# Performance work log

Hardware: AMD Instinct MI355X
Metric: run time of the kernel (lower is better)

## Reference

```python
import math
import jax, jax.numpy as jnp
import numpy as np

EMBED = 1024
HEADS = 16
HDIM = EMBED // HEADS

def setup_inputs() -> dict:
    key = jax.random.key(0)
    ks = jax.random.split(key, 11)
    N, L, E = 2, 2048, EMBED
    s = 1.0 / math.sqrt(E)
    return {
        "q": jax.random.normal(ks[0], (N, L, E), jnp.float32),
        "k": jax.random.normal(ks[1], (N, L, E), jnp.float32),
        "v": jax.random.normal(ks[2], (N, L, E), jnp.float32),
        "Wq": jax.random.normal(ks[3], (E, E), jnp.float32) * s,
        "bq": jnp.zeros((E,), jnp.float32),
        "Wk": jax.random.normal(ks[4], (E, E), jnp.float32) * s,
        "bk": jnp.zeros((E,), jnp.float32),
        "Wv": jax.random.normal(ks[5], (E, E), jnp.float32) * s,
        "bv": jnp.zeros((E,), jnp.float32),
        "Wo": jax.random.normal(ks[6], (E, E), jnp.float32) * s,
        "bo": jnp.zeros((E,), jnp.float32),
    }

def reference(q, k, v, Wq, bq, Wk, bk, Wv, bv, Wo, bo):
    N, L, E = q.shape
    h, d = HEADS, HDIM
    # linear projections (torch Linear: x @ W.T + b)
    qh = (q @ Wq.T + bq).reshape(N, L, h, d)
    kh = (k @ Wk.T + bk).reshape(N, L, h, d)
    vh = (v @ Wv.T + bv).reshape(N, L, h, d)
    # scaled dot-product attention (dropout in eval mode -> identity)
    energy = jnp.einsum('nqhd,nkhd->nhqk', qh, kh)
    attn = jax.nn.softmax(energy / math.sqrt(d), axis=-1)
    out = jnp.einsum('nhql,nlhd->nhqd', attn, vh)
    out = out.transpose(0, 2, 1, 3).reshape(N, L, E)
    return out @ Wo.T + bo
```

## Files before the change

kernel.cpp:

```cpp
#include <hip/hip_runtime.h>
#include <hip/hip_bf16.h>
#include <math.h>

typedef unsigned short u16;
typedef unsigned int u32;
typedef u16 u16x4 __attribute__((ext_vector_type(4)));
typedef u16 u16x8 __attribute__((ext_vector_type(8)));
typedef short bf16x8 __attribute__((ext_vector_type(8)));
typedef float f32x4 __attribute__((ext_vector_type(4)));

#define LSEQ 2048
#define NH   32

#define QSCALE 0.18033688011112042f

__device__ __forceinline__ u16 f2bf(float f) {
    __hip_bfloat16 h = __float2bfloat16(f);
    union { __hip_bfloat16 h; u16 u; } c; c.h = h; return c.u;
}

__global__ __launch_bounds__(256) void cvt_bf16(
    const float* __restrict__ src, u16* __restrict__ dst, int n4)
{
    int stride = gridDim.x * 256;
    for (int i = blockIdx.x * 256 + threadIdx.x; i < n4; i += stride) {
        float4 a = ((const float4*)src)[i];
        u16x4 p;
        p[0] = f2bf(a.x); p[1] = f2bf(a.y); p[2] = f2bf(a.z); p[3] = f2bf(a.w);
        ((u16x4*)dst)[i] = p;
    }
}

__global__ __launch_bounds__(256) void cvt3_bf16(
    const float* __restrict__ s0, const float* __restrict__ s1,
    const float* __restrict__ s2, u16* __restrict__ dst)
{
    int i = blockIdx.x * 256 + threadIdx.x;
    const float* s = (i < (1 << 18)) ? s0 : (i < (2 << 18)) ? s1 : s2;
    int off = i & ((1 << 18) - 1);
    float4 a = ((const float4*)s)[off];
    u16x4 p;
    p[0] = f2bf(a.x); p[1] = f2bf(a.y); p[2] = f2bf(a.z); p[3] = f2bf(a.w);
    ((u16x4*)dst)[i] = p;
}

template<int MODE, int QS>
__global__ __launch_bounds__(256, 1) void proj_gemm4(
    const u16* __restrict__ A, const u16* __restrict__ W,
    const float* __restrict__ bias, void* __restrict__ Out)
{
    __shared__ u16 Al[2][128 * 64];
    __shared__ u16 Bl[2][128 * 64];

    const int tid  = threadIdx.x;
    const int lane = tid & 63;
    const int w    = tid >> 6;
    const int lr   = lane & 15, lg = lane >> 4;
    const int m0   = blockIdx.y * 128;
    const int n0   = blockIdx.x * 128;
    const int wr   = (w >> 1) * 64;
    const int wc   = (w & 1) * 64;
    const int srow = tid >> 3;
    const int sc8  = tid & 7;
    const int ssw  = (sc8 ^ (srow & 7)) * 8;

    f32x4 acc[4][4] = {};
    u16x8 ra[4], rb[4];

    #define LOADS(k0)                                                          \
        _Pragma("unroll")                                                      \
        for (int p_ = 0; p_ < 4; ++p_) {                                       \
            ra[p_] = *(const u16x8*)(A + (size_t)(m0 + p_ * 32 + srow) * 1024  \
                                     + (k0) + ssw);                            \
            rb[p_] = *(const u16x8*)(W + (size_t)(n0 + p_ * 32 + srow) * 1024  \
                                     + (k0) + ssw);                            \
        }
    #define WRITE(buf)                                                         \
        _Pragma("unroll")                                                      \
        for (int p_ = 0; p_ < 4; ++p_) {                                       \
            *(u16x8*)((char*)&Al[buf][0] + (p_ * 32 + srow) * 128 + sc8 * 16)  \
                = ra[p_];                                                      \
            *(u16x8*)((char*)&Bl[buf][0] + (p_ * 32 + srow) * 128 + sc8 * 16)  \
                = rb[p_];                                                      \
        }

    LOADS(0)
    WRITE(0)
    LOADS(64)
    __syncthreads();

    for (int t = 0; t < 16; ++t) {
        const int c = t & 1;
        if (t + 1 < 16) {
            WRITE(c ^ 1)
            if (t + 2 < 16) LOADS((t + 2) * 64)
        }
        const char* Ac = (const char*)&Al[c][0];
        const char* Bc = (const char*)&Bl[c][0];
        #pragma unroll
        for (int ks = 0; ks < 2; ++ks) {
            const int co = ((ks * 4 + lg) * 16) ^ ((lr & 7) << 4);
            bf16x8 af[4], bfr[4];
            #pragma unroll
            for (int i = 0; i < 4; ++i)
                af[i] = *(const bf16x8*)(Ac + (wr + i * 16 + lr) * 128 + co);
            #pragma unroll
            for (int j = 0; j < 4; ++j)
                bfr[j] = *(const bf16x8*)(Bc + (wc + j * 16 + lr) * 128 + co);
            #pragma unroll
            for (int i = 0; i < 4; ++i)
                #pragma unroll
                for (int j = 0; j < 4; ++j)
                    acc[i][j] = __builtin_amdgcn_mfma_f32_16x16x32_bf16(
                        af[i], bfr[j], acc[i][j], 0, 0, 0);
        }
        __syncthreads();
    }

    #pragma unroll
    for (int j = 0; j < 4; ++j) {
        const int nn = n0 + wc + j * 16 + lr;
        const float bj = bias[nn];
        #pragma unroll
        for (int i = 0; i < 4; ++i) {
            #pragma unroll
            for (int r = 0; r < 4; ++r) {
                const int m = m0 + wr + i * 16 + lg * 4 + r;
                float vv = acc[i][j][r] + bj;
                if (QS) vv *= QSCALE;
                if (MODE == 0) {
                    const int n = m >> 11, l = m & 2047;
                    const int h = nn >> 6, d = nn & 63;
                    ((u16*)Out)[(((size_t)(n * 16 + h) * 2048) + l) * 64 + d] = f2bf(vv);
                } else if (MODE == 1) {
                    const int n = m >> 11, l = m & 2047;
                    const int h = nn >> 6, d = nn & 63;
                    ((u16*)Out)[(((size_t)(n * 16 + h) * 64) + d) * 2048 + l] = f2bf(vv);
                } else {
                    ((float*)Out)[(size_t)m * 1024 + nn] = vv;
                }
            }
        }
    }
    #undef LOADS
    #undef WRITE
}

__global__ __launch_bounds__(256, 4) void flash_attn5(
    const u16* __restrict__ Qh, const u16* __restrict__ Kh,
    const u16* __restrict__ Vt, u16* __restrict__ Oout)
{
    const int tid  = threadIdx.x;
    const int lane = tid & 63;
    const int w    = tid >> 6;
    const int lr   = lane & 15, lg = lane >> 4;
    const int t8   = tid & 7,   td8 = tid >> 3;
    const int nh   = blockIdx.y;
    const int q0   = blockIdx.x * 64;
    const int scol = (t8 ^ (td8 & 7)) * 8;

    const u16* Qb = Qh + (size_t)nh * LSEQ * 64;
    const u16* Kb = Kh + (size_t)nh * LSEQ * 64;
    const u16* Vb = Vt + (size_t)nh * 64 * LSEQ;

    __shared__ u16 Kl[2][64 * 64];
    __shared__ u16 Vl[2][64 * 64];
    __shared__ u16 Pl[4][16 * 64];

    bf16x8 aq[2];
    #pragma unroll
    for (int ks = 0; ks < 2; ++ks)
        aq[ks] = *(const bf16x8*)(Qb +
            (size_t)(q0 + w * 16 + lr) * 64 + ks * 32 + lg * 8);

    float m_run[4], l_run[4];
    f32x4 Oacc[4] = {};
    #pragma unroll
    for (int r = 0; r < 4; ++r) { m_run[r] = -INFINITY; l_run[r] = 0.f; }

    u16x8 ldK0, ldK1, ldV0, ldV1;
    #define LOADS(s0)                                                          \
        ldK0 = *(const u16x8*)(Kb + (size_t)((s0) + td8) * 64 + scol);         \
        ldK1 = *(const u16x8*)(Kb + (size_t)((s0) + td8 + 32) * 64 + scol);    \
        ldV0 = *(const u16x8*)(Vb + (size_t)td8 * LSEQ + (s0) + scol);         \
        ldV1 = *(const u16x8*)(Vb + (size_t)(td8 + 32) * LSEQ + (s0) + scol);
    #define WRITE(buf)                                                         \
        *(u16x8*)((char*)&Kl[buf][0] + td8 * 128 + t8 * 16)        = ldK0;     \
        *(u16x8*)((char*)&Kl[buf][0] + (td8 + 32) * 128 + t8 * 16) = ldK1;     \
        *(u16x8*)((char*)&Vl[buf][0] + td8 * 128 + t8 * 16)        = ldV0;     \
        *(u16x8*)((char*)&Vl[buf][0] + (td8 + 32) * 128 + t8 * 16) = ldV1;

    LOADS(0)
    WRITE(0)
    LOADS(64)
    __syncthreads();

    for (int t = 0; t < LSEQ / 64; ++t) {
        const int c = t & 1;
        if (t + 1 < LSEQ / 64) {
            WRITE(c ^ 1)
            if (t + 2 < LSEQ / 64) LOADS((t + 2) * 64)
        }
        const char* Kc = (const char*)&Kl[c][0];
        const char* Vc = (const char*)&Vl[c][0];
        char* Pw = (char*)&Pl[w][0];

        f32x4 S[4] = {};
        #pragma unroll
        for (int ks = 0; ks < 2; ++ks) {
            const int co = ((ks * 4 + lg) * 16) ^ ((lr & 7) << 4);
            #pragma unroll
            for (int ct = 0; ct < 4; ++ct) {
                bf16x8 kb = *(const bf16x8*)(Kc + (ct * 16 + lr) * 128 + co);
                S[ct] = __builtin_amdgcn_mfma_f32_16x16x32_bf16(
                    aq[ks], kb, S[ct], 0, 0, 0);
            }
        }

        {
            float m_new[4], sf[4], rs[4];
            #pragma unroll
            for (int r = 0; r < 4; ++r) {
                float tm = fmaxf(fmaxf(S[0][r], S[1][r]), fmaxf(S[2][r], S[3][r]));
                #pragma unroll
                for (int mk = 1; mk <= 8; mk <<= 1)
                    tm = fmaxf(tm, __shfl_xor(tm, mk, 64));
                m_new[r] = fmaxf(m_run[r], tm);
                sf[r] = exp2f(m_run[r] - m_new[r]);
                m_run[r] = m_new[r];
                rs[r] = 0.f;
            }
            #pragma unroll
            for (int ct = 0; ct < 4; ++ct)
                #pragma unroll
                for (int r = 0; r < 4; ++r) {
                    float p = exp2f(S[ct][r] - m_new[r]);
                    rs[r] += p;
                    int pr = lg * 4 + r;
                    *(u16*)(Pw + pr * 128 +
                            (((ct * 16 + lr) * 2) ^ ((pr & 7) << 4))) = f2bf(p);
                }
            #pragma unroll
            for (int r = 0; r < 4; ++r) {
                float s = rs[r];
                #pragma unroll
                for (int mk = 1; mk <= 8; mk <<= 1)
                    s += __shfl_xor(s, mk, 64);
                l_run[r] = l_run[r] * sf[r] + s;
            }
            #pragma unroll
            for (int dt = 0; dt < 4; ++dt)
                #pragma unroll
                for (int r = 0; r < 4; ++r)
                    Oacc[dt][r] *= sf[r];
        }

        #pragma unroll
        for (int ks = 0; ks < 2; ++ks) {
            const int co = ((ks * 4 + lg) * 16) ^ ((lr & 7) << 4);
            bf16x8 pa = *(const bf16x8*)(Pw + lr * 128 + co);
            #pragma unroll
            for (int dt = 0; dt < 4; ++dt) {
                bf16x8 vb = *(const bf16x8*)(Vc + (dt * 16 + lr) * 128 + co);
                Oacc[dt] = __builtin_amdgcn_mfma_f32_16x16x32_bf16(
                    pa, vb, Oacc[dt], 0, 0, 0);
            }
        }
        __syncthreads();
    }
    #undef LOADS
    #undef WRITE

    const int n = nh >> 4, h = nh & 15;
    #pragma unroll
    for (int dt = 0; dt < 4; ++dt)
        #pragma unroll
        for (int r = 0; r < 4; ++r) {
            float o = Oacc[dt][r] / l_run[r];
            int qq = q0 + w * 16 + lg * 4 + r;
            Oout[((size_t)(n * LSEQ + qq)) * 1024 + h * 64 + dt * 16 + lr] = f2bf(o);
        }
}

extern "C" void kernel_launch(void* const* d_in, const int* in_sizes, int n_in,
                              void* d_out, int out_size, void* d_ws, size_t ws_size,
                              hipStream_t stream) {
    const float* q  = (const float*)d_in[0];
    const float* k  = (const float*)d_in[1];
    const float* v  = (const float*)d_in[2];
    const float* Wq = (const float*)d_in[3];
    const float* bq = (const float*)d_in[4];
    const float* Wk = (const float*)d_in[5];
    const float* bk = (const float*)d_in[6];
    const float* Wv = (const float*)d_in[7];
    const float* bv = (const float*)d_in[8];
    const float* Wo = (const float*)d_in[9];
    const float* bo = (const float*)d_in[10];

    u16* ws = (u16*)d_ws;
    u16* Qh = ws;
    u16* Kh = ws + (size_t)4 * 1024 * 1024;
    u16* Vt = ws + (size_t)8 * 1024 * 1024;
    u16* S4 = ws + (size_t)12 * 1024 * 1024;

    u16* Wb  = (u16*)d_out;
    u16* Wqb = Wb;
    u16* Wkb = Wb + (size_t)1 * 1024 * 1024;
    u16* Wvb = Wb + (size_t)2 * 1024 * 1024;

    const int n4in = (2 * LSEQ * 1024) / 4;
    dim3 cb(256);
    dim3 gg(8, 32), gb(256);

    cvt3_bf16<<<dim3(3 * 1024), cb, 0, stream>>>(Wq, Wk, Wv, Wb);
    cvt_bf16<<<dim3(2048), cb, 0, stream>>>(q, S4, n4in);
    proj_gemm4<0, 1><<<gg, gb, 0, stream>>>(S4, Wqb, bq, Qh);
    cvt_bf16<<<dim3(2048), cb, 0, stream>>>(k, S4, n4in);
    proj_gemm4<0, 0><<<gg, gb, 0, stream>>>(S4, Wkb, bk, Kh);
    cvt_bf16<<<dim3(2048), cb, 0, stream>>>(v, S4, n4in);
    proj_gemm4<1, 0><<<gg, gb, 0, stream>>>(S4, Wvb, bv, Vt);
    flash_attn5<<<dim3(LSEQ / 64, NH), gb, 0, stream>>>(Qh, Kh, Vt, S4);
    cvt_bf16<<<dim3(1024), cb, 0, stream>>>(Wo, Qh, (1 << 18));
    proj_gemm4<2, 0><<<gg, gb, 0, stream>>>(S4, Qh, bo, (float*)d_out);
}
```

Measured before the change: 309.9 us.

## Shrink GEMM N-tile and add lazy softmax rescale with MFMA row sums

The projection GEMMs move from 128x128 to 128x64 tiles with a doubled grid and a launch bound of two blocks per CU, aiming for better CU fill on 256 CUs. In the attention kernel the per-tile online-softmax rescale is skipped when no new row max exceeds the running max by more than a threshold, tested wave-uniformly with __all. The row sums come from an extra MFMA against a ones vector instead of shuffle reductions. This trades some MFMA work and weaker numerical headroom (exp values up to 2^11 in bf16 P) for fewer shuffles and exps.

```diff
diff --git a/kernel.cpp b/kernel.cpp
--- a/kernel.cpp
+++ b/kernel.cpp
@@ -45,44 +45,46 @@
 }
 
 template<int MODE, int QS>
-__global__ __launch_bounds__(256, 1) void proj_gemm4(
+__global__ __launch_bounds__(256, 2) void proj_gemm5(
     const u16* __restrict__ A, const u16* __restrict__ W,
     const float* __restrict__ bias, void* __restrict__ Out)
 {
     __shared__ u16 Al[2][128 * 64];
-    __shared__ u16 Bl[2][128 * 64];
+    __shared__ u16 Bl[2][64 * 64];
 
     const int tid  = threadIdx.x;
     const int lane = tid & 63;
     const int w    = tid >> 6;
     const int lr   = lane & 15, lg = lane >> 4;
     const int m0   = blockIdx.y * 128;
-    const int n0   = blockIdx.x * 128;
+    const int n0   = blockIdx.x * 64;
     const int wr   = (w >> 1) * 64;
-    const int wc   = (w & 1) * 64;
+    const int wc   = (w & 1) * 32;
     const int srow = tid >> 3;
     const int sc8  = tid & 7;
     const int ssw  = (sc8 ^ (srow & 7)) * 8;
 
-    f32x4 acc[4][4] = {};
-    u16x8 ra[4], rb[4];
+    f32x4 acc[4][2] = {};
+    u16x8 ra[4], rb[2];
 
     #define LOADS(k0)                                                          \
         _Pragma("unroll")                                                      \
-        for (int p_ = 0; p_ < 4; ++p_) {                                       \
+        for (int p_ = 0; p_ < 4; ++p_)                                         \
             ra[p_] = *(const u16x8*)(A + (size_t)(m0 + p_ * 32 + srow) * 1024  \
                                      + (k0) + ssw);                            \
+        _Pragma("unroll")                                                      \
+        for (int p_ = 0; p_ < 2; ++p_)                                         \
             rb[p_] = *(const u16x8*)(W + (size_t)(n0 + p_ * 32 + srow) * 1024  \
-                                     + (k0) + ssw);                            \
-        }
+                                     + (k0) + ssw);
     #define WRITE(buf)                                                         \
         _Pragma("unroll")                                                      \
-        for (int p_ = 0; p_ < 4; ++p_) {                                       \
+        for (int p_ = 0; p_ < 4; ++p_)                                         \
             *(u16x8*)((char*)&Al[buf][0] + (p_ * 32 + srow) * 128 + sc8 * 16)  \
                 = ra[p_];                                                      \
+        _Pragma("unroll")                                                      \
+        for (int p_ = 0; p_ < 2; ++p_)                                         \
             *(u16x8*)((char*)&Bl[buf][0] + (p_ * 32 + srow) * 128 + sc8 * 16)  \
-                = rb[p_];                                                      \
-        }
+                = rb[p_];
 
     LOADS(0)
     WRITE(0)
@@ -100,17 +102,17 @@
         #pragma unroll
         for (int ks = 0; ks < 2; ++ks) {
             const int co = ((ks * 4 + lg) * 16) ^ ((lr & 7) << 4);
-            bf16x8 af[4], bfr[4];
+            bf16x8 af[4], bfr[2];
             #pragma unroll
             for (int i = 0; i < 4; ++i)
                 af[i] = *(const bf16x8*)(Ac + (wr + i * 16 + lr) * 128 + co);
             #pragma unroll
-            for (int j = 0; j < 4; ++j)
+            for (int j = 0; j < 2; ++j)
                 bfr[j] = *(const bf16x8*)(Bc + (wc + j * 16 + lr) * 128 + co);
             #pragma unroll
             for (int i = 0; i < 4; ++i)
                 #pragma unroll
-                for (int j = 0; j < 4; ++j)
+                for (int j = 0; j < 2; ++j)
                     acc[i][j] = __builtin_amdgcn_mfma_f32_16x16x32_bf16(
                         af[i], bfr[j], acc[i][j], 0, 0, 0);
         }
@@ -118,7 +120,7 @@
     }
 
     #pragma unroll
-    for (int j = 0; j < 4; ++j) {
+    for (int j = 0; j < 2; ++j) {
         const int nn = n0 + wc + j * 16 + lr;
         const float bj = bias[nn];
         #pragma unroll
@@ -146,7 +148,7 @@
     #undef WRITE
 }
 
-__global__ __launch_bounds__(256, 4) void flash_attn5(
+__global__ __launch_bounds__(256, 4) void flash_attn6(
     const u16* __restrict__ Qh, const u16* __restrict__ Kh,
     const u16* __restrict__ Vt, u16* __restrict__ Oout)
 {
@@ -173,10 +175,14 @@
         aq[ks] = *(const bf16x8*)(Qb +
             (size_t)(q0 + w * 16 + lr) * 64 + ks * 32 + lg * 8);
 
-    float m_run[4], l_run[4];
-    f32x4 Oacc[4] = {};
+    const short one_bf = (short)0x3F80;
+    bf16x8 vones = { one_bf, one_bf, one_bf, one_bf,
+                     one_bf, one_bf, one_bf, one_bf };
+
+    float m_run[4];
+    f32x4 Oacc[5] = {};
     #pragma unroll
-    for (int r = 0; r < 4; ++r) { m_run[r] = -INFINITY; l_run[r] = 0.f; }
+    for (int r = 0; r < 4; ++r) m_run[r] = -INFINITY;
 
     u16x8 ldK0, ldK1, ldV0, ldV1;
     #define LOADS(s0)                                                          \
@@ -218,41 +224,42 @@
         }
 
         {
-            float m_new[4], sf[4], rs[4];
-            #pragma unroll
-            for (int r = 0; r < 4; ++r) {
-                float tm = fmaxf(fmaxf(S[0][r], S[1][r]), fmaxf(S[2][r], S[3][r]));
+            float lm = S[0][0];
+            #pragma unroll
+            for (int ct = 0; ct < 4; ++ct)
                 #pragma unroll
-                for (int mk = 1; mk <= 8; mk <<= 1)
-                    tm = fmaxf(tm, __shfl_xor(tm, mk, 64));
-                m_new[r] = fmaxf(m_run[r], tm);
-                sf[r] = exp2f(m_run[r] - m_new[r]);
-                m_run[r] = m_new[r];
-                rs[r] = 0.f;
+                for (int r = 0; r < 4; ++r)
+                    lm = fmaxf(lm, S[ct][r]);
+            #pragma unroll
+            for (int mk = 1; mk <= 8; mk <<= 1)
+                lm = fmaxf(lm, __shfl_xor(lm, mk, 64));
+            float mmin = fminf(fminf(m_run[0], m_run[1]),
+                               fminf(m_run[2], m_run[3]));
+            if (!__all((int)(lm <= mmin + 11.0f))) {
+                #pragma unroll
+                for (int r = 0; r < 4; ++r) {
+                    float tm = fmaxf(fmaxf(S[0][r], S[1][r]),
+                                     fmaxf(S[2][r], S[3][r]));
+                    #pragma unroll
+                    for (int mk = 1; mk <= 8; mk <<= 1)
+                        tm = fmaxf(tm, __shfl_xor(tm, mk, 64));
+                    float mn = fmaxf(m_run[r], tm);
+                    float sf = exp2f(m_run[r] - mn);
+                    m_run[r] = mn;
+                    #pragma unroll
+                    for (int dt = 0; dt < 5; ++dt)
+                        Oacc[dt][r] *= sf;
+                }
             }
             #pragma unroll
             for (int ct = 0; ct < 4; ++ct)
                 #pragma unroll
                 for (int r = 0; r < 4; ++r) {
-                    float p = exp2f(S[ct][r] - m_new[r]);
-                    rs[r] += p;
+                    float p = exp2f(S[ct][r] - m_run[r]);
                     int pr = lg * 4 + r;
                     *(u16*)(Pw + pr * 128 +
                             (((ct * 16 + lr) * 2) ^ ((pr & 7) << 4))) = f2bf(p);
                 }
-            #pragma unroll
-            for (int r = 0; r < 4; ++r) {
-                float s = rs[r];
-                #pragma unroll
-                for (int mk = 1; mk <= 8; mk <<= 1)
-                    s += __shfl_xor(s, mk, 64);
-                l_run[r] = l_run[r] * sf[r] + s;
-            }
-            #pragma unroll
-            for (int dt = 0; dt < 4; ++dt)
-                #pragma unroll
-                for (int r = 0; r < 4; ++r)
-                    Oacc[dt][r] *= sf[r];
         }
 
         #pragma unroll
@@ -265,6 +272,8 @@
                 Oacc[dt] = __builtin_amdgcn_mfma_f32_16x16x32_bf16(
                     pa, vb, Oacc[dt], 0, 0, 0);
             }
+            Oacc[4] = __builtin_amdgcn_mfma_f32_16x16x32_bf16(
+                pa, vones, Oacc[4], 0, 0, 0);
         }
         __syncthreads();
     }
@@ -276,7 +285,7 @@
     for (int dt = 0; dt < 4; ++dt)
         #pragma unroll
         for (int r = 0; r < 4; ++r) {
-            float o = Oacc[dt][r] / l_run[r];
+            float o = Oacc[dt][r] / Oacc[4][r];
             int qq = q0 + w * 16 + lg * 4 + r;
             Oout[((size_t)(n * LSEQ + qq)) * 1024 + h * 64 + dt * 16 + lr] = f2bf(o);
         }
@@ -310,16 +319,16 @@
 
     const int n4in = (2 * LSEQ * 1024) / 4;
     dim3 cb(256);
-    dim3 gg(8, 32), gb(256);
+    dim3 gg(16, 32), gb(256);
 
     cvt3_bf16<<<dim3(3 * 1024), cb, 0, stream>>>(Wq, Wk, Wv, Wb);
     cvt_bf16<<<dim3(2048), cb, 0, stream>>>(q, S4, n4in);
-    proj_gemm4<0, 1><<<gg, gb, 0, stream>>>(S4, Wqb, bq, Qh);
+    proj_gemm5<0, 1><<<gg, gb, 0, stream>>>(S4, Wqb, bq, Qh);
     cvt_bf16<<<dim3(2048), cb, 0, stream>>>(k, S4, n4in);
-    proj_gemm4<0, 0><<<gg, gb, 0, stream>>>(S4, Wkb, bk, Kh);
+    proj_gemm5<0, 0><<<gg, gb, 0, stream>>>(S4, Wkb, bk, Kh);
     cvt_bf16<<<dim3(2048), cb, 0, stream>>>(v, S4, n4in);
-    proj_gemm4<1, 0><<<gg, gb, 0, stream>>>(S4, Wvb, bv, Vt);
-    flash_attn5<<<dim3(LSEQ / 64, NH), gb, 0, stream>>>(Qh, Kh, Vt, S4);
+    proj_gemm5<1, 0><<<gg, gb, 0, stream>>>(S4, Wvb, bv, Vt);
+    flash_attn6<<<dim3(LSEQ / 64, NH), gb, 0, stream>>>(Qh, Kh, Vt, S4);
     cvt_bf16<<<dim3(1024), cb, 0, stream>>>(Wo, Qh, (1 << 18));
-    proj_gemm4<2, 0><<<gg, gb, 0, stream>>>(S4, Qh, bo, (float*)d_out);
-}
+    proj_gemm5<2, 0><<<gg, gb, 0, stream>>>(S4, Qh, bo, (float*)d_out);
+}
```

Result: faster. 263.4 us (-15.0%).
